# Kernel tuning notes

Hardware: AMD Instinct MI355X
Metric: run time of the kernel (lower is better)

## Reference

```python
import jax, jax.numpy as jnp
import numpy as np

B, N, C, H, D, K = 4, 8192, 384, 12, 2, 256
M = N // K          # 32 members per cluster
CH = C // H         # 32 head dim


def setup_inputs() -> dict:
    key = jax.random.key(0)
    ks = jax.random.split(key, 8)
    pos = jax.random.uniform(ks[0], (B, N, D), jnp.float32) * 100.0
    feat = jax.random.normal(ks[1], (B, N, C), jnp.float32)
    # each batch's points partitioned into K clusters of M members (a permutation)
    perms = jax.vmap(lambda kk: jax.random.permutation(kk, N))(jax.random.split(ks[2], B))
    member_idx = perms.reshape(B * K, M).astype(jnp.int32)               # z x m
    batch_idx = jnp.broadcast_to(
        jnp.repeat(jnp.arange(B, dtype=jnp.int32), K)[:, None], (B * K, M))
    w = 0.02
    qkv_w = jax.random.normal(ks[3], (3 * C, C), jnp.float32) * w
    qkv_b = jnp.zeros((3 * C,), jnp.float32)
    pos_w = jax.random.normal(ks[4], (H, D), jnp.float32) * w
    pos_b = jnp.zeros((H,), jnp.float32)
    proj_w = jax.random.normal(ks[5], (C, C), jnp.float32) * w
    proj_b = jnp.zeros((C,), jnp.float32)
    return dict(pos=pos, feat=feat, member_idx=member_idx, batch_idx=batch_idx,
                qkv_w=qkv_w, qkv_b=qkv_b, pos_w=pos_w, pos_b=pos_b,
                proj_w=proj_w, proj_b=proj_b, k=K)


def reference(pos, feat, member_idx, batch_idx, qkv_w, qkv_b, pos_w, pos_b,
              proj_w, proj_b, k):
    # attend_means=True, mask=None, cluster_score=None, q_subsample_idx=None path
    b, n, c = feat.shape
    d = pos.shape[2]
    h = pos_w.shape[0]
    ch = c // h
    z, m = member_idx.shape
    scale = ch ** -0.5

    qkv = feat @ qkv_w.T + qkv_b            # b,n,3c
    q = qkv[..., :c]                        # b,n,c
    kv = qkv[..., c:]                       # b,n,2c

    pos_orig = pos
    pos_n = pos / jnp.max(pos.reshape(-1, d), axis=0)   # per-coordinate max norm

    # irregular gather of kv / pos per cluster member
    kv_g = kv[batch_idx, member_idx]        # z,m,2c
    pos_g = pos_n[batch_idx, member_idx]    # z,m,d

    # cluster_score=None, mask=None -> uniform weights 1/m (mean over members)
    kv_mean = jnp.mean(kv_g, axis=1).reshape(b, k, 2, h, ch)
    pos_mean = jnp.mean(pos_g, axis=1).reshape(b, k, d)

    key_ = kv_mean[:, :, 0].transpose(0, 2, 1, 3)   # b,h,k,ch
    v = kv_mean[:, :, 1].transpose(0, 2, 1, 3)      # b,h,k,ch
    qh = q.reshape(b, n, h, ch).transpose(0, 2, 1, 3) * scale  # b,h,n,ch

    attn = jnp.einsum('bhnc,bhkc->bhnk', qh, key_)  # b,h,n,k
    rel_pos = pos_mean[:, None, :, :] - pos_orig[:, :, None, :]  # b,n,k,d
    pos_bias = jnp.einsum('bnkd,hd->bhnk', rel_pos, pos_w) + pos_b[None, :, None, None]
    attn = jax.nn.softmax(attn + pos_bias, axis=-1)

    out = jnp.einsum('bhnk,bhkc->bnhc', attn, v).reshape(b, n, c)
    return out @ proj_w.T + proj_b
```

## Files before the change

kernel.cpp:

```cpp
#include <hip/hip_runtime.h>

typedef __attribute__((ext_vector_type(8))) short bf16x8;
typedef __attribute__((ext_vector_type(4))) float f32x4;

#define MFMA16(a,b,c) __builtin_amdgcn_mfma_f32_16x16x32_bf16((a),(b),(c),0,0,0)

__device__ __forceinline__ float b2f(unsigned short u){
  union { unsigned u; float f; } x; x.u = ((unsigned)u) << 16; return x.f;
}
__device__ __forceinline__ unsigned short f2b(float f){
  union { float f; unsigned u; } x; x.f = f;
  unsigned r = x.u + 0x7FFFu + ((x.u >> 16) & 1u);
  return (unsigned short)(r >> 16);
}
__device__ __forceinline__ unsigned pk_rne(float a, float b){
  unsigned ua = __float_as_uint(a), ub = __float_as_uint(b);
  ua += 0x7FFFu + ((ua >> 16) & 1u);
  ub += 0x7FFFu + ((ub >> 16) & 1u);
  return __builtin_amdgcn_perm(ub, ua, 0x07060302u);
}
__device__ __forceinline__ unsigned pk_trunc(float a, float b){
  return __builtin_amdgcn_perm(__float_as_uint(b), __float_as_uint(a), 0x07060302u);
}
__device__ __forceinline__ bf16x8 mk8(unsigned a, unsigned b, unsigned c, unsigned d){
  union { uint4 u; bf16x8 h; } x; x.u = make_uint4(a,b,c,d); return x.h;
}
__device__ __forceinline__ int permp(int cl){
  return (cl & 0xE0) | (((cl >> 2) & 3) << 3) | (((cl >> 4) & 1) << 2) | (cl & 3);
}

typedef __attribute__((address_space(3))) unsigned int lds_u32;
typedef const __attribute__((address_space(1))) unsigned int glb_u32;
__device__ __forceinline__ void gl_lds16(const void* g, void* l){
  __builtin_amdgcn_global_load_lds((glb_u32*)g, (lds_u32*)l, 16, 0, 0);
}

__global__ __launch_bounds__(256) void prep_kernel(
    const float* __restrict__ pos, unsigned* __restrict__ pmax,
    const float* __restrict__ qkv_w, unsigned short* __restrict__ qkvwb,
    const float* __restrict__ proj_w, unsigned short* __restrict__ projwb)
{
  int bid = blockIdx.x, tid = threadIdx.x;
  if (bid < 64){
    int i = bid*256 + tid;
    float4 v = ((const float4*)pos)[i];
    float m0 = fmaxf(v.x, v.z), m1 = fmaxf(v.y, v.w);
    #pragma unroll
    for (int off = 32; off >= 1; off >>= 1){
      m0 = fmaxf(m0, __shfl_xor(m0, off, 64));
      m1 = fmaxf(m1, __shfl_xor(m1, off, 64));
    }
    if ((tid & 63) == 0){
      atomicMax(&pmax[0], __float_as_uint(m0));
      atomicMax(&pmax[1], __float_as_uint(m1));
    }
  } else {
    const float* in; unsigned short* o; long i;
    if (bid < 280){ in = qkv_w;  o = qkvwb;  i = (long)(bid-64)*256 + tid; }
    else          { in = proj_w; o = projwb; i = (long)(bid-280)*256 + tid; }
    const float4* p = (const float4*)(in + i*8);
    float4 a = p[0], b = p[1];
    *(uint4*)(o + i*8) = make_uint4(pk_rne(a.x,a.y), pk_rne(a.z,a.w),
                                    pk_rne(b.x,b.y), pk_rne(b.z,b.w));
  }
}

__global__ __launch_bounds__(192) void cluster_means_kernel(
    const float* __restrict__ feat, const float* __restrict__ pos,
    const int* __restrict__ member_idx, const int* __restrict__ batch_idx,
    unsigned short* __restrict__ fm, float* __restrict__ pm)
{
  int t = threadIdx.x;
  int g = t / 96, tl = t - g*96;
  int z = blockIdx.x*2 + g;
  __shared__ int bases[2][32];
  if (tl < 32) bases[g][tl] = batch_idx[z*32 + tl]*8192 + member_idx[z*32 + tl];
  __syncthreads();
  float4 a = {0.f,0.f,0.f,0.f};
  float p = 0.f;
  const float4* f4 = (const float4*)feat;
  #pragma unroll 8
  for (int m = 0; m < 32; m++){
    int row = bases[g][m];
    float4 v = f4[(long)row*96 + tl];
    a.x += v.x; a.y += v.y; a.z += v.z; a.w += v.w;
    if (tl < 2) p += pos[(long)row*2 + tl];
  }
  unsigned d0 = pk_rne(a.x*(1.f/32.f), a.y*(1.f/32.f));
  unsigned d1 = pk_rne(a.z*(1.f/32.f), a.w*(1.f/32.f));
  *(uint2*)(fm + (long)z*384 + tl*4) = make_uint2(d0, d1);
  if (tl < 2) pm[z*2 + tl] = p * (1.f/32.f);
}

__global__ __launch_bounds__(256) void bias_kernel(
    const float* __restrict__ pm, const float* __restrict__ pmaxf,
    const float* __restrict__ pos_w, const float* __restrict__ pos_b,
    unsigned short* __restrict__ wt)
{
  int idx = blockIdx.x*256 + threadIdx.x;
  int kc = idx & 255;
  int bh = idx >> 8;
  int h = bh % 12;
  float p0 = pm[((bh/12)*256 + kc)*2]   / pmaxf[0];
  float p1 = pm[((bh/12)*256 + kc)*2+1] / pmaxf[1];
  float bias = p0*pos_w[h*2] + p1*pos_w[h*2+1] + pos_b[h];
  wt[(bh << 8) + permp(kc)] = f2b(exp2f(bias * 1.44269504088896340f));
}

__global__ __launch_bounds__(256) void gemm_kv_kernel(
    const unsigned short* __restrict__ A, const unsigned short* __restrict__ W,
    const float* __restrict__ bias, unsigned short* __restrict__ kh,
    unsigned short* __restrict__ vt, const unsigned short* __restrict__ wt)
{
  __shared__ unsigned short As[64*64];
  __shared__ unsigned short Ws[128*64];
  const int N = 768, K = 384;
  int mt = blockIdx.x / 6, nt = blockIdx.x - mt*6;
  int m0 = mt << 6, n0 = nt << 7;
  int tid = threadIdx.x;
  int lane = tid & 63, wave = tid >> 6;
  int wr = (wave >> 1) << 5, wc = (wave & 1) << 6;
  int l15 = lane & 15, quad = lane >> 4;
  int sw = l15 & 7;
  int srow = tid >> 3, sc8 = tid & 7;

  f32x4 acc[2][4];
  #pragma unroll
  for (int i = 0; i < 2; i++)
    #pragma unroll
    for (int j = 0; j < 4; j++) acc[i][j] = (f32x4){0.f,0.f,0.f,0.f};

  for (int k0 = 0; k0 < K; k0 += 64){
    __syncthreads();
    #pragma unroll
    for (int it = 0; it < 2; it++){
      int r = srow + it*32;
      int gc8 = sc8 ^ (r & 7);
      gl_lds16(A + (long)(m0+r)*K + k0 + gc8*8, As + it*2048 + wave*512);
    }
    #pragma unroll
    for (int it = 0; it < 4; it++){
      int r = srow + it*32;
      int gc8 = sc8 ^ (r & 7);
      gl_lds16(W + (long)(n0+r)*K + k0 + gc8*8, Ws + it*2048 + wave*512);
    }
    __syncthreads();
    #pragma unroll
    for (int kk = 0; kk < 2; kk++){
      bf16x8 af[2], bfr[4];
      #pragma unroll
      for (int i = 0; i < 2; i++)
        af[i] = *(const bf16x8*)(As + (wr + i*16 + l15)*64 + (((kk<<2)+quad) ^ sw)*8);
      #pragma unroll
      for (int j = 0; j < 4; j++)
        bfr[j] = *(const bf16x8*)(Ws + (wc + j*16 + l15)*64 + (((kk<<2)+quad) ^ sw)*8);
      #pragma unroll
      for (int i = 0; i < 2; i++)
        #pragma unroll
        for (int j = 0; j < 4; j++)
          acc[i][j] = MFMA16(af[i], bfr[j], acc[i][j]);
    }
  }

  #pragma unroll
  for (int j = 0; j < 4; j++){
    int col = n0 + wc + j*16 + l15;
    float bv = bias[col];
    #pragma unroll
    for (int i = 0; i < 2; i++){
      int row0 = m0 + wr + i*16 + quad*4;
      #pragma unroll
      for (int r = 0; r < 4; r++){
        float v = acc[i][j][r] + bv;
        int row = row0 + r;
        int b = row >> 8, cl = row & 255;
        if (col < 384){
          int h = col >> 5, ch = col & 31;
          kh[((((long)b*12 + h)*256 + cl)*32) + ch] = f2b(v);
        } else {
          int cn = col - 384;
          int h = cn >> 5, ch = cn & 31;
          int pp = permp(cl);
          int c8 = (pp >> 3) ^ (ch & 7);
          float w = b2f(wt[(((long)b*12 + h) << 8) + pp]);
          vt[(((long)b*12 + h)*32 + ch)*256 + c8*8 + (pp & 7)] = f2b(v * w);
        }
      }
    }
  }
}

template<int OUT_F32, int AF32, int AHM, int CHM>
__global__ __launch_bounds__(512) void gemm_fn_kernel(
    const void* __restrict__ Av, const unsigned short* __restrict__ W,
    const float* __restrict__ bias, void* __restrict__ Cv, float out_scale)
{
  __shared__ unsigned short As[64*72];
  __shared__ unsigned short Ws[384*64];
  const int K = 384, N = 384;
  int m0 = blockIdx.x << 6;
  int tid = threadIdx.x;
  int lane = tid & 63, wave = tid >> 6;
  int l15 = lane & 15, quad = lane >> 4;
  int sw = l15 & 7;
  int srow = tid >> 3, sc8 = tid & 7;

  f32x4 acc[4][3];
  #pragma unroll
  for (int i = 0; i < 4; i++)
    #pragma unroll
    for (int j = 0; j < 3; j++) acc[i][j] = (f32x4){0.f,0.f,0.f,0.f};

  for (int k0 = 0; k0 < K; k0 += 64){
    __syncthreads();
    if (AF32){
      const float* Af = (const float*)Av;
      const float4* src = (const float4*)(Af + (long)(m0+srow)*K + k0 + sc8*8);
      float4 v0 = src[0], v1 = src[1];
      *(uint4*)(As + srow*72 + sc8*8) = make_uint4(pk_rne(v0.x,v0.y), pk_rne(v0.z,v0.w),
                                                   pk_rne(v1.x,v1.y), pk_rne(v1.z,v1.w));
    } else {
      const unsigned short* A = (const unsigned short*)Av;
      int gc8 = sc8 ^ (srow & 7);
      const unsigned short* src;
      if (AHM){
        int row = m0 + srow;
        int bb = row >> 13, tok = row & 8191;
        int ch = k0 + gc8*8;
        src = A + ((((long)(bb*12 + (ch >> 5))) << 13) + tok)*32 + (ch & 31);
      } else {
        src = A + (long)(m0+srow)*K + k0 + gc8*8;
      }
      gl_lds16(src, As + wave*512);
    }
    #pragma unroll
    for (int it = 0; it < 6; it++){
      int r = it*64 + srow;
      int gc8 = sc8 ^ (r & 7);
      gl_lds16(W + (long)r*K + k0 + gc8*8, Ws + it*4096 + wave*512);
    }
    __syncthreads();
    #pragma unroll
    for (int kk = 0; kk < 2; kk++){
      bf16x8 af[4];
      #pragma unroll
      for (int i = 0; i < 4; i++){
        int r = i*16 + l15;
        if (AF32) af[i] = *(const bf16x8*)(As + r*72 + ((kk<<2)+quad)*8);
        else      af[i] = *(const bf16x8*)(As + r*64 + (((kk<<2)+quad) ^ sw)*8);
      }
      #pragma unroll
      for (int j = 0; j < 3; j++){
        bf16x8 bfr = *(const bf16x8*)(Ws + (wave*48 + j*16 + l15)*64 + (((kk<<2)+quad) ^ sw)*8);
        #pragma unroll
        for (int i = 0; i < 4; i++)
          acc[i][j] = MFMA16(af[i], bfr, acc[i][j]);
      }
    }
  }

  #pragma unroll
  for (int j = 0; j < 3; j++){
    int col = wave*48 + j*16 + l15;
    float bv = bias[col];
    #pragma unroll
    for (int i = 0; i < 4; i++){
      int row0 = m0 + i*16 + quad*4;
      #pragma unroll
      for (int r = 0; r < 4; r++){
        float v = (acc[i][j][r] + bv) * out_scale;
        int row = row0 + r;
        if (OUT_F32){
          ((float*)Cv)[(long)row*N + col] = v;
        } else if (CHM){
          int bb = row >> 13, tok = row & 8191;
          ((unsigned short*)Cv)[((((long)(bb*12 + (col >> 5))) << 13) + tok)*32 + (col & 31)] = f2b(v);
        } else {
          ((unsigned short*)Cv)[(long)row*N + col] = f2b(v);
        }
      }
    }
  }
}

__global__ __launch_bounds__(256) void attn_kernel(
    const unsigned short* __restrict__ qhm,
    const unsigned short* __restrict__ kh,
    const unsigned short* __restrict__ vt,
    const unsigned short* __restrict__ wt,
    unsigned short* __restrict__ aohm)
{
  __shared__ unsigned short keyS[256*32];
  __shared__ unsigned short vTS[32*256];
  __shared__ unsigned short wS[256];

  int bid = blockIdx.x;
  int chunk = bid & 63;
  int bh = bid >> 6;
  int n0 = chunk << 7;
  int tid = threadIdx.x, lane = tid & 63, wave = tid >> 6;
  int l15 = lane & 15, quad = lane >> 4;
  int sw = l15 & 7;

  const unsigned short* khb = kh + (long)bh*8192;
  const unsigned short* vtb = vt + (long)bh*8192;
  #pragma unroll
  for (int it = 0; it < 4; it++){
    gl_lds16(khb + it*2048 + tid*8, keyS + it*2048 + wave*512);
    gl_lds16(vtb + it*2048 + tid*8, vTS  + it*2048 + wave*512);
  }
  if (tid < 32) *(uint4*)(wS + tid*8) = *(const uint4*)(wt + ((long)bh << 8) + tid*8);

  long qbase = ((long)bh*8192 + n0 + wave*32 + l15)*32 + quad*8;
  bf16x8 aq0 = *(const bf16x8*)(qhm + qbase);
  bf16x8 aq1 = *(const bf16x8*)(qhm + qbase + 512);
  __syncthreads();

  #pragma unroll
  for (int ti = 0; ti < 2; ti++){
    bf16x8 aq = ti ? aq1 : aq0;

    f32x4 S[16];
    #pragma unroll
    for (int kb = 0; kb < 16; kb++){
      bf16x8 bk = *(const bf16x8*)(keyS + (kb*16 + l15)*32 + quad*8);
      f32x4 z = {0.f,0.f,0.f,0.f};
      S[kb] = MFMA16(bk, aq, z);
    }

    #pragma unroll
    for (int kb = 0; kb < 16; kb++)
      #pragma unroll
      for (int c = 0; c < 4; c++) S[kb][c] = exp2f(S[kb][c]);

    f32x4 o0 = {0.f,0.f,0.f,0.f}, o1 = {0.f,0.f,0.f,0.f}, os = {0.f,0.f,0.f,0.f};
    #pragma unroll
    for (int ks = 0; ks < 8; ks++){
      bf16x8 pf = mk8(pk_trunc(S[2*ks][0],   S[2*ks][1]),
                      pk_trunc(S[2*ks][2],   S[2*ks][3]),
                      pk_trunc(S[2*ks+1][0], S[2*ks+1][1]),
                      pk_trunc(S[2*ks+1][2], S[2*ks+1][3]));
      int c8 = (4*ks + quad) ^ sw;
      bf16x8 a0 = *(const bf16x8*)(vTS + l15*256      + c8*8);
      bf16x8 a1 = *(const bf16x8*)(vTS + (16+l15)*256 + c8*8);
      bf16x8 wf = *(const bf16x8*)(wS + ks*32 + quad*8);
      o0 = MFMA16(a0, pf, o0);
      o1 = MFMA16(a1, pf, o1);
      os = MFMA16(wf, pf, os);
    }
    float inv = 1.f / os[0];
    long obase = ((long)bh*8192 + n0 + wave*32 + ti*16 + l15)*32 + quad*4;
    unsigned q0 = pk_rne(o0[0]*inv, o0[1]*inv), q1 = pk_rne(o0[2]*inv, o0[3]*inv);
    unsigned q2 = pk_rne(o1[0]*inv, o1[1]*inv), q3 = pk_rne(o1[2]*inv, o1[3]*inv);
    *(uint2*)(aohm + obase)      = make_uint2(q0, q1);
    *(uint2*)(aohm + obase + 16) = make_uint2(q2, q3);
  }
}

extern "C" void kernel_launch(void* const* d_in, const int* in_sizes, int n_in,
                              void* d_out, int out_size, void* d_ws, size_t ws_size,
                              hipStream_t stream)
{
  const float* pos      = (const float*)d_in[0];
  const float* feat     = (const float*)d_in[1];
  const int* member_idx = (const int*)d_in[2];
  const int* batch_idx  = (const int*)d_in[3];
  const float* qkv_w    = (const float*)d_in[4];
  const float* qkv_b    = (const float*)d_in[5];
  const float* pos_w    = (const float*)d_in[6];
  const float* pos_b    = (const float*)d_in[7];
  const float* proj_w   = (const float*)d_in[8];
  const float* proj_b   = (const float*)d_in[9];
  float* out = (float*)d_out;

  char* ws = (char*)d_ws;
  float* pmax           = (float*)ws;
  float* pm             = (float*)(ws + 256);
  unsigned short* fm    = (unsigned short*)(ws + 8704);
  unsigned short* kh    = (unsigned short*)(ws + 795136);
  unsigned short* vt    = (unsigned short*)(ws + 1581568);
  unsigned short* wt    = (unsigned short*)(ws + 2368000);
  unsigned short* q_s   = (unsigned short*)(ws + 2417152);
  unsigned short* ao    = (unsigned short*)(ws + 27582976);
  unsigned short* qkvwb = (unsigned short*)(ws + 52748800);
  unsigned short* projwb= (unsigned short*)(ws + 53633536);

  hipMemsetAsync(pmax, 0, 8, stream);
  prep_kernel<<<352, 256, 0, stream>>>(pos, (unsigned*)pmax, qkv_w, qkvwb, proj_w, projwb);
  cluster_means_kernel<<<512, 192, 0, stream>>>(feat, pos, member_idx, batch_idx, fm, pm);
  bias_kernel<<<48, 256, 0, stream>>>(pm, pmax, pos_w, pos_b, wt);
  gemm_kv_kernel<<<96, 256, 0, stream>>>(fm, qkvwb + 384*384, qkv_b + 384, kh, vt, wt);
  gemm_fn_kernel<0,1,0,1><<<512, 512, 0, stream>>>(feat, qkvwb, qkv_b, q_s,
                                                   0.17677669529663687f * 1.44269504088896340f);
  attn_kernel<<<3072, 256, 0, stream>>>(q_s, kh, vt, wt, ao);
  gemm_fn_kernel<1,0,1,0><<<512, 512, 0, stream>>>(ao, projwb, proj_b, out, 1.0f);
}
```

Measured before the change: 221.6 us.

## Emit bf16 features from cluster-means pass and interleave attention row tiles

```diff
diff --git a/kernel.cpp b/kernel.cpp
--- a/kernel.cpp
+++ b/kernel.cpp
@@ -68,7 +68,8 @@
 __global__ __launch_bounds__(192) void cluster_means_kernel(
     const float* __restrict__ feat, const float* __restrict__ pos,
     const int* __restrict__ member_idx, const int* __restrict__ batch_idx,
-    unsigned short* __restrict__ fm, float* __restrict__ pm)
+    unsigned short* __restrict__ fm, float* __restrict__ pm,
+    unsigned short* __restrict__ featb)
 {
   int t = threadIdx.x;
   int g = t / 96, tl = t - g*96;
@@ -83,6 +84,7 @@
   for (int m = 0; m < 32; m++){
     int row = bases[g][m];
     float4 v = f4[(long)row*96 + tl];
+    *(uint2*)(featb + (long)row*384 + tl*4) = make_uint2(pk_rne(v.x,v.y), pk_rne(v.z,v.w));
     a.x += v.x; a.y += v.y; a.z += v.z; a.w += v.w;
     if (tl < 2) p += pos[(long)row*2 + tl];
   }
@@ -316,45 +318,55 @@
   bf16x8 aq1 = *(const bf16x8*)(qhm + qbase + 512);
   __syncthreads();
 
-  #pragma unroll
-  for (int ti = 0; ti < 2; ti++){
-    bf16x8 aq = ti ? aq1 : aq0;
-
-    f32x4 S[16];
-    #pragma unroll
-    for (int kb = 0; kb < 16; kb++){
-      bf16x8 bk = *(const bf16x8*)(keyS + (kb*16 + l15)*32 + quad*8);
-      f32x4 z = {0.f,0.f,0.f,0.f};
-      S[kb] = MFMA16(bk, aq, z);
-    }
-
-    #pragma unroll
-    for (int kb = 0; kb < 16; kb++)
-      #pragma unroll
-      for (int c = 0; c < 4; c++) S[kb][c] = exp2f(S[kb][c]);
-
-    f32x4 o0 = {0.f,0.f,0.f,0.f}, o1 = {0.f,0.f,0.f,0.f}, os = {0.f,0.f,0.f,0.f};
-    #pragma unroll
-    for (int ks = 0; ks < 8; ks++){
-      bf16x8 pf = mk8(pk_trunc(S[2*ks][0],   S[2*ks][1]),
-                      pk_trunc(S[2*ks][2],   S[2*ks][3]),
-                      pk_trunc(S[2*ks+1][0], S[2*ks+1][1]),
-                      pk_trunc(S[2*ks+1][2], S[2*ks+1][3]));
-      int c8 = (4*ks + quad) ^ sw;
-      bf16x8 a0 = *(const bf16x8*)(vTS + l15*256      + c8*8);
-      bf16x8 a1 = *(const bf16x8*)(vTS + (16+l15)*256 + c8*8);
-      bf16x8 wf = *(const bf16x8*)(wS + ks*32 + quad*8);
-      o0 = MFMA16(a0, pf, o0);
-      o1 = MFMA16(a1, pf, o1);
-      os = MFMA16(wf, pf, os);
-    }
-    float inv = 1.f / os[0];
-    long obase = ((long)bh*8192 + n0 + wave*32 + ti*16 + l15)*32 + quad*4;
-    unsigned q0 = pk_rne(o0[0]*inv, o0[1]*inv), q1 = pk_rne(o0[2]*inv, o0[3]*inv);
-    unsigned q2 = pk_rne(o1[0]*inv, o1[1]*inv), q3 = pk_rne(o1[2]*inv, o1[3]*inv);
-    *(uint2*)(aohm + obase)      = make_uint2(q0, q1);
-    *(uint2*)(aohm + obase + 16) = make_uint2(q2, q3);
-  }
+  bf16x8 pf0[8], pf1[8];
+  #pragma unroll
+  for (int ks = 0; ks < 8; ks++){
+    bf16x8 bk0 = *(const bf16x8*)(keyS + ((2*ks  )*16 + l15)*32 + quad*8);
+    bf16x8 bk1 = *(const bf16x8*)(keyS + ((2*ks+1)*16 + l15)*32 + quad*8);
+    f32x4 z = {0.f,0.f,0.f,0.f};
+    f32x4 s00 = MFMA16(bk0, aq0, z);
+    f32x4 s01 = MFMA16(bk1, aq0, z);
+    f32x4 s10 = MFMA16(bk0, aq1, z);
+    f32x4 s11 = MFMA16(bk1, aq1, z);
+    #pragma unroll
+    for (int c = 0; c < 4; c++){
+      s00[c] = exp2f(s00[c]); s01[c] = exp2f(s01[c]);
+      s10[c] = exp2f(s10[c]); s11[c] = exp2f(s11[c]);
+    }
+    pf0[ks] = mk8(pk_trunc(s00[0],s00[1]), pk_trunc(s00[2],s00[3]),
+                  pk_trunc(s01[0],s01[1]), pk_trunc(s01[2],s01[3]));
+    pf1[ks] = mk8(pk_trunc(s10[0],s10[1]), pk_trunc(s10[2],s10[3]),
+                  pk_trunc(s11[0],s11[1]), pk_trunc(s11[2],s11[3]));
+  }
+
+  f32x4 o00 = {0.f,0.f,0.f,0.f}, o01 = {0.f,0.f,0.f,0.f}, os0 = {0.f,0.f,0.f,0.f};
+  f32x4 o10 = {0.f,0.f,0.f,0.f}, o11 = {0.f,0.f,0.f,0.f}, os1 = {0.f,0.f,0.f,0.f};
+  #pragma unroll
+  for (int ks = 0; ks < 8; ks++){
+    int c8 = (4*ks + quad) ^ sw;
+    bf16x8 a0 = *(const bf16x8*)(vTS + l15*256      + c8*8);
+    bf16x8 a1 = *(const bf16x8*)(vTS + (16+l15)*256 + c8*8);
+    bf16x8 wf = *(const bf16x8*)(wS + ks*32 + quad*8);
+    o00 = MFMA16(a0, pf0[ks], o00);
+    o01 = MFMA16(a1, pf0[ks], o01);
+    os0 = MFMA16(wf, pf0[ks], os0);
+    o10 = MFMA16(a0, pf1[ks], o10);
+    o11 = MFMA16(a1, pf1[ks], o11);
+    os1 = MFMA16(wf, pf1[ks], os1);
+  }
+
+  float inv0 = 1.f / os0[0];
+  float inv1 = 1.f / os1[0];
+  long ob0 = ((long)bh*8192 + n0 + wave*32 + l15)*32 + quad*4;
+  *(uint2*)(aohm + ob0)      = make_uint2(pk_rne(o00[0]*inv0, o00[1]*inv0),
+                                          pk_rne(o00[2]*inv0, o00[3]*inv0));
+  *(uint2*)(aohm + ob0 + 16) = make_uint2(pk_rne(o01[0]*inv0, o01[1]*inv0),
+                                          pk_rne(o01[2]*inv0, o01[3]*inv0));
+  long ob1 = ob0 + 512;
+  *(uint2*)(aohm + ob1)      = make_uint2(pk_rne(o10[0]*inv1, o10[1]*inv1),
+                                          pk_rne(o10[2]*inv1, o10[3]*inv1));
+  *(uint2*)(aohm + ob1 + 16) = make_uint2(pk_rne(o11[0]*inv1, o11[1]*inv1),
+                                          pk_rne(o11[2]*inv1, o11[3]*inv1));
 }
 
 extern "C" void kernel_launch(void* const* d_in, const int* in_sizes, int n_in,
@@ -384,13 +396,14 @@
   unsigned short* ao    = (unsigned short*)(ws + 27582976);
   unsigned short* qkvwb = (unsigned short*)(ws + 52748800);
   unsigned short* projwb= (unsigned short*)(ws + 53633536);
+  unsigned short* featb = (unsigned short*)(ws + 53928448);
 
   hipMemsetAsync(pmax, 0, 8, stream);
   prep_kernel<<<352, 256, 0, stream>>>(pos, (unsigned*)pmax, qkv_w, qkvwb, proj_w, projwb);
-  cluster_means_kernel<<<512, 192, 0, stream>>>(feat, pos, member_idx, batch_idx, fm, pm);
+  cluster_means_kernel<<<512, 192, 0, stream>>>(feat, pos, member_idx, batch_idx, fm, pm, featb);
   bias_kernel<<<48, 256, 0, stream>>>(pm, pmax, pos_w, pos_b, wt);
   gemm_kv_kernel<<<96, 256, 0, stream>>>(fm, qkvwb + 384*384, qkv_b + 384, kh, vt, wt);
-  gemm_fn_kernel<0,1,0,1><<<512, 512, 0, stream>>>(feat, qkvwb, qkv_b, q_s,
+  gemm_fn_kernel<0,0,0,1><<<512, 512, 0, stream>>>(featb, qkvwb, qkv_b, q_s,
                                                    0.17677669529663687f * 1.44269504088896340f);
   attn_kernel<<<3072, 256, 0, stream>>>(q_s, kh, vt, wt, ao);
   gemm_fn_kernel<1,0,1,0><<<512, 512, 0, stream>>>(ao, projwb, proj_b, out, 1.0f);
```

Result: slower. 227.2 us (+2.5%).
